# Kernel tuning notes

Measured on AMD Instinct MI355X. Metric: run time of the kernel, lower is better.

## Reference

```python
import jax, jax.numpy as jnp
import numpy as np

HIDDEN = 2048
NH = 32        # query heads
NKV = 4        # kv heads (GQA)
HD = 64        # head_dim
Q_SIZE = NH * HD      # 2048
KV_SIZE = NKV * HD    # 256
WINDOW = 1024         # sliding window size
THETA = 1000000.0
T = 2048              # tokens
SCALE = HD ** -0.5
NEG = -1e30


def setup_inputs() -> dict:
    key = jax.random.key(0)
    k1, k2, k3 = jax.random.split(key, 3)
    return {
        "positions": jnp.arange(T, dtype=jnp.int32),
        "hidden_states": jax.random.normal(k1, (T, HIDDEN), dtype=jnp.float32),
        "wqkv": jax.random.normal(k2, (HIDDEN, Q_SIZE + 2 * KV_SIZE), dtype=jnp.float32) * (HIDDEN ** -0.5),
        "wo": jax.random.normal(k3, (Q_SIZE, HIDDEN), dtype=jnp.float32) * (Q_SIZE ** -0.5),
    }


def _apply_rope(x, positions):
    # NeoX-style rotary embedding over full head_dim (rotate halves).
    half = HD // 2
    inv_freq = 1.0 / (THETA ** (jnp.arange(half, dtype=jnp.float32) / half))
    ang = positions.astype(jnp.float32)[:, None] * inv_freq[None, :]   # [T, half]
    cos = jnp.cos(ang)[:, None, :]   # [T, 1, half]
    sin = jnp.sin(ang)[:, None, :]
    x1, x2 = jnp.split(x, 2, axis=-1)
    return jnp.concatenate([x1 * cos - x2 * sin, x2 * cos + x1 * sin], axis=-1)


def reference(positions, hidden_states, wqkv, wo):
    # fused QKV projection
    qkv = hidden_states @ wqkv                          # [T, Q+2KV]
    q = qkv[:, :Q_SIZE].reshape(T, NH, HD)
    k = qkv[:, Q_SIZE:Q_SIZE + KV_SIZE].reshape(T, NKV, HD)
    v = qkv[:, Q_SIZE + KV_SIZE:].reshape(T, NKV, HD)
    # rotary embedding on q, k
    q = _apply_rope(q, positions)
    k = _apply_rope(k, positions)
    # GQA: repeat kv heads to match query heads
    group = NH // NKV
    kr = jnp.repeat(k, group, axis=1)                   # [T, NH, HD]
    vr = jnp.repeat(v, group, axis=1)
    scores = jnp.einsum('qhd,khd->hqk', q, kr) * SCALE  # [NH, T, T]
    # causal + sliding-window mask: attend to j in (i-WINDOW, i]
    i = jnp.arange(T)[:, None]
    j = jnp.arange(T)[None, :]
    mask = (j <= i) & (i - j < WINDOW)                  # [T, T]
    scores = jnp.where(mask[None, :, :], scores, NEG)
    probs = jax.nn.softmax(scores, axis=-1)
    attn = jnp.einsum('hqk,khd->qhd', probs, vr).reshape(T, Q_SIZE)
    return attn @ wo                                    # [T, HIDDEN]
```

## Files before the change

### kernel.cpp

```cpp
#include <hip/hip_runtime.h>
#include <hip/hip_bf16.h>

typedef float  f32x4  __attribute__((ext_vector_type(4)));
typedef __bf16 bf16x8 __attribute__((ext_vector_type(8)));
typedef __bf16 bf16x4 __attribute__((ext_vector_type(4)));
typedef __bf16 bf16x2 __attribute__((ext_vector_type(2)));

#define T_SEQ   2048
#define HIDDEN  2048
#define NH      32
#define NKV     4
#define HD      64
#define QSZ     2048
#define KVSZ    256
#define QKVN    2560
#define WINDOW  1024

#if __has_builtin(__builtin_amdgcn_exp2f)
#define EXPS(x) __builtin_amdgcn_exp2f(x)
#define QSCALE  0.1803368801111f
#else
#define EXPS(x) __expf(x)
#define QSCALE  0.125f
#endif

__device__ __forceinline__ void gll16(const __bf16* g, __bf16* l) {
    __builtin_amdgcn_global_load_lds(
        (const __attribute__((address_space(1))) void*)g,
        (__attribute__((address_space(3))) void*)l,
        16, 0, 0);
}

__global__ __launch_bounds__(256) void cvt_f32_bf16(const float4* __restrict__ in,
                                                    bf16x4* __restrict__ out) {
    int id = blockIdx.x * 256 + threadIdx.x;
    float4 v = in[id];
    bf16x4 o;
    o[0] = (__bf16)v.x; o[1] = (__bf16)v.y; o[2] = (__bf16)v.z; o[3] = (__bf16)v.w;
    out[id] = o;
}

__global__ __launch_bounds__(256) void transpose_f32_bf16(const float* __restrict__ in,
                                                          __bf16* __restrict__ out,
                                                          int Rin, int Cin) {
    __shared__ float tile[32][33];
    int r = threadIdx.x >> 5;
    int c = threadIdx.x & 31;
    int ri = blockIdx.y * 32, ci = blockIdx.x * 32;
    #pragma unroll
    for (int i = 0; i < 4; i++)
        tile[r + i*8][c] = in[(size_t)(ri + r + i*8) * Cin + ci + c];
    __syncthreads();
    #pragma unroll
    for (int i = 0; i < 4; i++)
        out[(size_t)(ci + r + i*8) * Rin + ri + c] = (__bf16)tile[c][r + i*8];
}


#define GEMM_PROLOGUE(Aptr, Btptr, Kdim)                                        \
    __shared__ __align__(16) __bf16 Asm[2][64 * 64];                            \
    __shared__ __align__(16) __bf16 Bsm[2][128 * 64];                           \
    const int tid = threadIdx.x;                                                \
    const int wid = tid >> 6;                                                   \
    const int l   = tid & 63;                                                   \
    const int lg  = l >> 4;                                                     \
    const int ll  = l & 15;                                                     \
    const int swl = ll & 7;                                                     \
    const int wm  = wid >> 1, wn = wid & 1;                                     \
    const int gx   = gridDim.x;                                                 \
    const int flat = blockIdx.y * gx + blockIdx.x;                              \
    const int nwg  = gx * gridDim.y;                                            \
    const int swz  = (flat & 7) * (nwg >> 3) + (flat >> 3);                     \
    const int bm   = (swz / gx) * 64;                                           \
    const int bn   = (swz % gx) * 128;                                          \
    const __bf16* Ab = (Aptr) + (size_t)bm * (Kdim);                            \
    const __bf16* Bb = (Btptr) + (size_t)bn * (Kdim);                           \
    f32x4 acc[2][4];                                                            \
    _Pragma("unroll")                                                           \
    for (int i = 0; i < 2; i++)                                                 \
        _Pragma("unroll")                                                       \
        for (int j = 0; j < 4; j++)                                             \
            acc[i][j] = (f32x4){0.f, 0.f, 0.f, 0.f};                            \
    const int srow = tid >> 3;                                                  \
    const int sseg0 = tid & 7;

#define GEMM_STAGE(buf, k0, Kdim)                                               \
    {                                                                           \
        _Pragma("unroll")                                                       \
        for (int c = 0; c < 2; c++) {                                           \
            int row  = c * 32 + srow;                                           \
            int sseg = sseg0 ^ (row & 7);                                       \
            gll16(Ab + (size_t)row * (Kdim) + (k0) + sseg * 8,                  \
                  &Asm[buf][(c * 256 + tid) * 8]);                              \
        }                                                                       \
        _Pragma("unroll")                                                       \
        for (int c = 0; c < 4; c++) {                                           \
            int row  = c * 32 + srow;                                           \
            int sseg = sseg0 ^ (row & 7);                                       \
            gll16(Bb + (size_t)row * (Kdim) + (k0) + sseg * 8,                  \
                  &Bsm[buf][(c * 256 + tid) * 8]);                              \
        }                                                                       \
    }

#define GEMM_KLOOP(Kdim)                                                        \
    GEMM_STAGE(0, 0, Kdim)                                                      \
    __syncthreads();                                                            \
    int cur = 0;                                                                \
    for (int k0 = 0; k0 < (Kdim); k0 += 64) {                                   \
        if (k0 + 64 < (Kdim)) GEMM_STAGE(cur ^ 1, k0 + 64, Kdim)                \
        _Pragma("unroll")                                                       \
        for (int ss = 0; ss < 2; ss++) {                                        \
            bf16x8 af[2], bfr[4];                                               \
            _Pragma("unroll")                                                   \
            for (int mi = 0; mi < 2; mi++) {                                    \
                int r = wm * 32 + mi * 16 + ll;                                 \
                int u = (ss * 4 + lg) ^ swl;                                    \
                af[mi] = *reinterpret_cast<const bf16x8*>(&Asm[cur][r * 64 + u * 8]); \
            }                                                                   \
            _Pragma("unroll")                                                   \
            for (int ni = 0; ni < 4; ni++) {                                    \
                int r = wn * 64 + ni * 16 + ll;                                 \
                int u = (ss * 4 + lg) ^ swl;                                    \
                bfr[ni] = *reinterpret_cast<const bf16x8*>(&Bsm[cur][r * 64 + u * 8]); \
            }                                                                   \
            _Pragma("unroll")                                                   \
            for (int mi = 0; mi < 2; mi++)                                      \
                _Pragma("unroll")                                               \
                for (int ni = 0; ni < 4; ni++)                                  \
                    acc[mi][ni] = __builtin_amdgcn_mfma_f32_16x16x32_bf16(      \
                        af[mi], bfr[ni], acc[mi][ni], 0, 0, 0);                 \
        }                                                                       \
        __syncthreads();                                                        \
        cur ^= 1;                                                               \
    }

__global__ __launch_bounds__(256) void gemm_out(const __bf16* __restrict__ A,
                                                const __bf16* __restrict__ Bt,
                                                float* __restrict__ Cout,
                                                int M, int N, int K) {
    GEMM_PROLOGUE(A, Bt, K)
    GEMM_KLOOP(K)
    #pragma unroll
    for (int mi = 0; mi < 2; mi++)
        #pragma unroll
        for (int ni = 0; ni < 4; ni++)
            #pragma unroll
            for (int r = 0; r < 4; r++) {
                int row = bm + wm*32 + mi*16 + lg*4 + r;
                int col = bn + wn*64 + ni*16 + ll;
                Cout[(size_t)row * N + col] = acc[mi][ni][r];
            }
}

__global__ __launch_bounds__(256) void gemm_qkv(const __bf16* __restrict__ A,
                                                const __bf16* __restrict__ Bt,
                                                const int* __restrict__ pos,
                                                __bf16* __restrict__ q,
                                                __bf16* __restrict__ k,
                                                __bf16* __restrict__ vT) {
    GEMM_PROLOGUE(A, Bt, HIDDEN)
    GEMM_KLOOP(HIDDEN)

    if (bn < QSZ + KVSZ) {
        const bool isq = (bn < QSZ);
        const float ifr0 = exp2f((float)ll * -0.62286151779138f);
        const float ifr1 = exp2f((float)(16 + ll) * -0.62286151779138f);
        #pragma unroll
        for (int mi = 0; mi < 2; mi++) {
            #pragma unroll
            for (int r = 0; r < 4; r++) {
                int row = bm + wm*32 + mi*16 + lg*4 + r;
                float p = (float)pos[row];
                #pragma unroll
                for (int ni = 0; ni < 2; ni++) {
                    float ang = p * (ni ? ifr1 : ifr0);
                    float sn, cs;
                    sincosf(ang, &sn, &cs);
                    float x1 = acc[mi][ni][r], x2 = acc[mi][ni + 2][r];
                    float o1 = x1 * cs - x2 * sn;
                    float o2 = x2 * cs + x1 * sn;
                    int col = bn + wn*64 + ni*16 + ll;
                    if (isq) {
                        q[(size_t)row * QSZ + col]      = (__bf16)(o1 * QSCALE);
                        q[(size_t)row * QSZ + col + 32] = (__bf16)(o2 * QSCALE);
                    } else {
                        k[(size_t)row * KVSZ + (col - QSZ)]      = (__bf16)o1;
                        k[(size_t)row * KVSZ + (col - QSZ) + 32] = (__bf16)o2;
                    }
                }
            }
        }
    } else {
        #pragma unroll
        for (int mi = 0; mi < 2; mi++) {
            int row0 = bm + wm*32 + mi*16 + lg*4;
            #pragma unroll
            for (int ni = 0; ni < 4; ni++) {
                int d = bn + wn*64 + ni*16 + ll - (QSZ + KVSZ);
                bf16x4 pk;
                #pragma unroll
                for (int r = 0; r < 4; r++) pk[r] = (__bf16)acc[mi][ni][r];
                *reinterpret_cast<bf16x4*>(&vT[(size_t)d * T_SEQ + row0]) = pk;
            }
        }
    }
}

__global__ __launch_bounds__(512) void attn_kernel(const __bf16* __restrict__ qg,
                                                   const __bf16* __restrict__ kgl,
                                                   const __bf16* __restrict__ vTg,
                                                   __bf16* __restrict__ og) {
    const int qb  = blockIdx.x;
    const int hp  = blockIdx.y;
    const int kvh = hp >> 2;
    const int tid = threadIdx.x;
    const int wid = tid >> 6;
    const int h   = hp * 2 + (wid >> 2);
    const int l   = tid & 63;
    const int lg  = l >> 4;
    const int ll  = l & 15;
    const int i0  = qb * 64;
    const int qw  = i0 + (wid & 3) * 16;
    const int qi  = qw + ll;

    __shared__ __align__(16) __bf16 Ksm[2][64 * 64];
    __shared__ __align__(16) __bf16 VTs[2][64 * 64];

    bf16x8 qf[2];
    {
        const __bf16* qp = qg + (size_t)(qw + ll) * QSZ + h * 64 + lg * 8;
        qf[0] = *reinterpret_cast<const bf16x8*>(qp);
        qf[1] = *reinterpret_cast<const bf16x8*>(qp + 32);
    }

    f32x4 o[4];
    #pragma unroll
    for (int dn = 0; dn < 4; dn++) o[dn] = (f32x4){0.f, 0.f, 0.f, 0.f};
    float l_run = 0.f;

    int jlo = i0 - (WINDOW - 1); if (jlo < 0) jlo = 0;
    int t0v = jlo & ~63;
    int tend = i0 + 64;

    const int srow = tid >> 3;
    const int sg   = (tid & 7) ^ (srow & 7);
    const int krow = (srow & 35) | ((srow & 8) << 1) | ((srow & 4) << 1) | ((srow & 16) >> 2);
    const __bf16* kp = kgl + (size_t)krow * KVSZ + kvh * 64 + sg * 8;
    const __bf16* vp = vTg + (size_t)(kvh * 64 + srow) * T_SEQ + sg * 8;

#define ASTAGE(buf, t)                                      \
    {                                                       \
        gll16(kp + (size_t)(t) * KVSZ, &Ksm[buf][tid * 8]); \
        gll16(vp + (t),                &VTs[buf][tid * 8]); \
    }

    ASTAGE(0, t0v);
    __syncthreads();

    const int swl = ll & 7;
    const int u0 = (lg ^ swl) * 8;
    const int u1 = ((4 + lg) ^ swl) * 8;

    int cur = 0;
    for (int t = t0v; t < tend; t += 64) {
        if (t + 64 < tend) ASTAGE(cur ^ 1, t + 64);

        bool active = (t <= qw + 15) && (t + 63 >= qw - (WINDOW - 1));
        if (active) {
            f32x4 sT[4];
            __builtin_amdgcn_s_setprio(1);
            #pragma unroll
            for (int kt = 0; kt < 4; kt++) {
                sT[kt] = (f32x4){0.f, 0.f, 0.f, 0.f};
                bf16x8 kf0 = *reinterpret_cast<const bf16x8*>(&Ksm[cur][kt*1024 + ll*64 + u0]);
                sT[kt] = __builtin_amdgcn_mfma_f32_16x16x32_bf16(kf0, qf[0], sT[kt], 0, 0, 0);
                bf16x8 kf1 = *reinterpret_cast<const bf16x8*>(&Ksm[cur][kt*1024 + ll*64 + u1]);
                sT[kt] = __builtin_amdgcn_mfma_f32_16x16x32_bf16(kf1, qf[1], sT[kt], 0, 0, 0);
            }
            __builtin_amdgcn_s_setprio(0);

            bool full = (t + 63 <= qw) && (t >= qw + 15 - (WINDOW - 1));
            float ts = 0.f;
            if (full) {
                #pragma unroll
                for (int kt = 0; kt < 4; kt++) {
                    #pragma unroll
                    for (int r = 0; r < 4; r++) {
                        float p = EXPS(sT[kt][r]);
                        sT[kt][r] = p;
                        ts += p;
                    }
                }
            } else {
                #pragma unroll
                for (int kt = 0; kt < 4; kt++) {
                    int jb = t + ((kt & 2) << 4) + ((kt & 1) << 2) + (lg << 3);
                    #pragma unroll
                    for (int r = 0; r < 4; r++) {
                        int j = jb + r;
                        bool ok = (j <= qi) && (qi - j < WINDOW);
                        float p = ok ? EXPS(sT[kt][r]) : 0.f;
                        sT[kt][r] = p;
                        ts += p;
                    }
                }
            }
            ts += __shfl_xor(ts, 16);
            ts += __shfl_xor(ts, 32);
            l_run += ts;

            __builtin_amdgcn_s_setprio(1);
            #pragma unroll
            for (int kt2 = 0; kt2 < 2; kt2++) {
                bf16x8 pa;
                #pragma unroll
                for (int r = 0; r < 4; r++) {
                    pa[r]     = (__bf16)sT[kt2*2][r];
                    pa[r + 4] = (__bf16)sT[kt2*2 + 1][r];
                }
                int uv = kt2 ? u1 : u0;
                #pragma unroll
                for (int dn = 0; dn < 4; dn++) {
                    bf16x8 vf = *reinterpret_cast<const bf16x8*>(&VTs[cur][dn*1024 + ll*64 + uv]);
                    o[dn] = __builtin_amdgcn_mfma_f32_16x16x32_bf16(pa, vf, o[dn], 0, 0, 0);
                }
            }
            __builtin_amdgcn_s_setprio(0);
        }
        __syncthreads();
        cur ^= 1;
    }
#undef ASTAGE

    float linv = 1.0f / l_run;
    float i0v = __shfl(linv, lg*4 + 0);
    float i1v = __shfl(linv, lg*4 + 1);
    float i2v = __shfl(linv, lg*4 + 2);
    float i3v = __shfl(linv, lg*4 + 3);
    #pragma unroll
    for (int dn = 0; dn < 4; dn++) {
        og[(size_t)(qw + lg*4 + 0) * QSZ + h*64 + dn*16 + ll] = (__bf16)(o[dn][0] * i0v);
        og[(size_t)(qw + lg*4 + 1) * QSZ + h*64 + dn*16 + ll] = (__bf16)(o[dn][1] * i1v);
        og[(size_t)(qw + lg*4 + 2) * QSZ + h*64 + dn*16 + ll] = (__bf16)(o[dn][2] * i2v);
        og[(size_t)(qw + lg*4 + 3) * QSZ + h*64 + dn*16 + ll] = (__bf16)(o[dn][3] * i3v);
    }
}

extern "C" void kernel_launch(void* const* d_in, const int* in_sizes, int n_in,
                              void* d_out, int out_size, void* d_ws, size_t ws_size,
                              hipStream_t stream) {
    const int*   positions = (const int*)d_in[0];
    const float* hidden    = (const float*)d_in[1];
    const float* wqkv      = (const float*)d_in[2];
    const float* wo        = (const float*)d_in[3];
    float* out = (float*)d_out;

    char* ws = (char*)d_ws;
    __bf16* hidden_bf = (__bf16*)(ws);
    __bf16* wqkv_t    = (__bf16*)(ws + 8388608);
    __bf16* wo_t      = (__bf16*)(ws + 18874368);
    __bf16* q_bf      = (__bf16*)(ws + 37748736);
    __bf16* k_bf      = (__bf16*)(ws + 46137344);
    __bf16* vT_bf     = (__bf16*)(ws + 47185920);
    __bf16* attn_bf   = (__bf16*)(ws + 48234496);

    cvt_f32_bf16<<<dim3((T_SEQ * HIDDEN) / 4 / 256), dim3(256), 0, stream>>>(
        (const float4*)hidden, (bf16x4*)hidden_bf);
    transpose_f32_bf16<<<dim3(QKVN / 32, HIDDEN / 32), dim3(256), 0, stream>>>(
        wqkv, wqkv_t, HIDDEN, QKVN);
    transpose_f32_bf16<<<dim3(HIDDEN / 32, QSZ / 32), dim3(256), 0, stream>>>(
        wo, wo_t, QSZ, HIDDEN);

    gemm_qkv<<<dim3(QKVN / 128, T_SEQ / 64), dim3(256), 0, stream>>>(
        hidden_bf, wqkv_t, positions, q_bf, k_bf, vT_bf);

    attn_kernel<<<dim3(T_SEQ / 64, 16), dim3(512), 0, stream>>>(
        q_bf, k_bf, vT_bf, attn_bf);

    gemm_out<<<dim3(HIDDEN / 128, T_SEQ / 64), dim3(256), 0, stream>>>(
        attn_bf, wo_t, out, T_SEQ, HIDDEN, QSZ);
}
```

Measured before the change: 113.4 us.

## Fuse preprocessing kernels into one launch, widen transpose, precompute RoPE table

Merges the hidden-state conversion and the two weight transposes into a single prep kernel, cutting two launches. The transpose now uses a 32x128 tile with float4 loads and bf16x4 stores instead of scalar accesses. The prep kernel also builds a per-token cos/sin table, so the QKV GEMM epilogue reads precomputed values instead of calling sincosf. This trades redundant transcendental work in the epilogue for an extra table write and read, and the padded 32x132 shared tile may cause some bank conflicts in the column-wise read.

```diff
diff --git a/kernel.cpp b/kernel.cpp
--- a/kernel.cpp
+++ b/kernel.cpp
@@ -31,29 +31,69 @@
         16, 0, 0);
 }
 
-__global__ __launch_bounds__(256) void cvt_f32_bf16(const float4* __restrict__ in,
-                                                    bf16x4* __restrict__ out) {
-    int id = blockIdx.x * 256 + threadIdx.x;
-    float4 v = in[id];
-    bf16x4 o;
-    o[0] = (__bf16)v.x; o[1] = (__bf16)v.y; o[2] = (__bf16)v.z; o[3] = (__bf16)v.w;
-    out[id] = o;
-}
-
-__global__ __launch_bounds__(256) void transpose_f32_bf16(const float* __restrict__ in,
-                                                          __bf16* __restrict__ out,
-                                                          int Rin, int Cin) {
-    __shared__ float tile[32][33];
-    int r = threadIdx.x >> 5;
-    int c = threadIdx.x & 31;
-    int ri = blockIdx.y * 32, ci = blockIdx.x * 32;
+__global__ __launch_bounds__(256) void prep(const float4* __restrict__ hidden4,
+                                            bf16x4* __restrict__ hidden_bf4,
+                                            const float* __restrict__ wqkv,
+                                            const float* __restrict__ wo,
+                                            __bf16* __restrict__ wqkv_t,
+                                            __bf16* __restrict__ wo_t,
+                                            const int* __restrict__ pos,
+                                            float2* __restrict__ ropetab) {
+    __shared__ float tile[32][132];
+    const int b = blockIdx.x;
+    const int tid = threadIdx.x;
+
+    if (b < 4096) {
+        int id = b * 256 + tid;
+        float4 v = hidden4[id];
+        bf16x4 o;
+        o[0] = (__bf16)v.x; o[1] = (__bf16)v.y; o[2] = (__bf16)v.z; o[3] = (__bf16)v.w;
+        hidden_bf4[id] = o;
+        return;
+    }
+    if (b < 4352) {
+        int id = (b - 4096) * 256 + tid;
+        int row = id >> 5, f = id & 31;
+        float p = (float)pos[row];
+        float ifr = exp2f((float)f * -0.62286151779138f);
+        float sn, cs;
+        sincosf(p * ifr, &sn, &cs);
+        ropetab[id] = make_float2(cs, sn);
+        return;
+    }
+
+    const float* in;
+    __bf16* out;
+    int Rin, Cin, bx, by;
+    if (b < 5632) {
+        int t = b - 4352;
+        in = wqkv; out = wqkv_t; Rin = 2048; Cin = 2560;
+        bx = t % 20; by = t / 20;
+    } else {
+        int t = b - 5632;
+        in = wo; out = wo_t; Rin = 2048; Cin = 2048;
+        bx = t % 16; by = t / 16;
+    }
+    const int ri = by * 32, ci = bx * 128;
+    const int r0 = tid >> 5;
+    const int c4 = tid & 31;
     #pragma unroll
-    for (int i = 0; i < 4; i++)
-        tile[r + i*8][c] = in[(size_t)(ri + r + i*8) * Cin + ci + c];
+    for (int i = 0; i < 4; i++) {
+        float4 v = *reinterpret_cast<const float4*>(
+            &in[(size_t)(ri + r0 + i * 8) * Cin + ci + c4 * 4]);
+        *reinterpret_cast<float4*>(&tile[r0 + i * 8][c4 * 4]) = v;
+    }
     __syncthreads();
+    const int c  = tid >> 3;
+    const int rb = tid & 7;
     #pragma unroll
-    for (int i = 0; i < 4; i++)
-        out[(size_t)(ci + r + i*8) * Rin + ri + c] = (__bf16)tile[c][r + i*8];
+    for (int j = 0; j < 4; j++) {
+        int cc = c + j * 32;
+        bf16x4 pk;
+        #pragma unroll
+        for (int i = 0; i < 4; i++) pk[i] = (__bf16)tile[rb * 4 + i][cc];
+        *reinterpret_cast<bf16x4*>(&out[(size_t)(ci + cc) * Rin + ri + rb * 4]) = pk;
+    }
 }
 
 
@@ -154,7 +194,7 @@
 
 __global__ __launch_bounds__(256) void gemm_qkv(const __bf16* __restrict__ A,
                                                 const __bf16* __restrict__ Bt,
-                                                const int* __restrict__ pos,
+                                                const float2* __restrict__ ropetab,
                                                 __bf16* __restrict__ q,
                                                 __bf16* __restrict__ k,
                                                 __bf16* __restrict__ vT) {
@@ -163,22 +203,18 @@
 
     if (bn < QSZ + KVSZ) {
         const bool isq = (bn < QSZ);
-        const float ifr0 = exp2f((float)ll * -0.62286151779138f);
-        const float ifr1 = exp2f((float)(16 + ll) * -0.62286151779138f);
         #pragma unroll
         for (int mi = 0; mi < 2; mi++) {
             #pragma unroll
             for (int r = 0; r < 4; r++) {
                 int row = bm + wm*32 + mi*16 + lg*4 + r;
-                float p = (float)pos[row];
+                const float2* tb = &ropetab[row * 32 + ll];
                 #pragma unroll
                 for (int ni = 0; ni < 2; ni++) {
-                    float ang = p * (ni ? ifr1 : ifr0);
-                    float sn, cs;
-                    sincosf(ang, &sn, &cs);
+                    float2 cssn = tb[ni * 16];
                     float x1 = acc[mi][ni][r], x2 = acc[mi][ni + 2][r];
-                    float o1 = x1 * cs - x2 * sn;
-                    float o2 = x2 * cs + x1 * sn;
+                    float o1 = x1 * cssn.x - x2 * cssn.y;
+                    float o2 = x2 * cssn.x + x1 * cssn.y;
                     int col = bn + wn*64 + ni*16 + ll;
                     if (isq) {
                         q[(size_t)row * QSZ + col]      = (__bf16)(o1 * QSCALE);
@@ -363,16 +399,14 @@
     __bf16* k_bf      = (__bf16*)(ws + 46137344);
     __bf16* vT_bf     = (__bf16*)(ws + 47185920);
     __bf16* attn_bf   = (__bf16*)(ws + 48234496);
-
-    cvt_f32_bf16<<<dim3((T_SEQ * HIDDEN) / 4 / 256), dim3(256), 0, stream>>>(
-        (const float4*)hidden, (bf16x4*)hidden_bf);
-    transpose_f32_bf16<<<dim3(QKVN / 32, HIDDEN / 32), dim3(256), 0, stream>>>(
-        wqkv, wqkv_t, HIDDEN, QKVN);
-    transpose_f32_bf16<<<dim3(HIDDEN / 32, QSZ / 32), dim3(256), 0, stream>>>(
-        wo, wo_t, QSZ, HIDDEN);
+    float2* ropetab   = (float2*)(ws + 56623104);
+
+    prep<<<dim3(6656), dim3(256), 0, stream>>>(
+        (const float4*)hidden, (bf16x4*)hidden_bf, wqkv, wo,
+        wqkv_t, wo_t, positions, ropetab);
 
     gemm_qkv<<<dim3(QKVN / 128, T_SEQ / 64), dim3(256), 0, stream>>>(
-        hidden_bf, wqkv_t, positions, q_bf, k_bf, vT_bf);
+        hidden_bf, wqkv_t, ropetab, q_bf, k_bf, vT_bf);
 
     attn_kernel<<<dim3(T_SEQ / 64, 16), dim3(512), 0, stream>>>(
         q_bf, k_bf, vT_bf, attn_bf);
```

Result: faster. 109.9 us (-3.1%).
